# Optimization experiments

Measured on AMD Instinct MI355X. Metric: run time of the kernel, lower is better.

Reference implementation:

```python
import jax, jax.numpy as jnp
import numpy as np

N_NODES = 100_000
N_EDGES = 1_600_000
F_IN, F_HID, F_OUT = 128, 64, 128


def setup_inputs() -> dict:
    key = jax.random.key(0)
    k_x, k_e, k_w1, k_w2 = jax.random.split(key, 4)
    x = jax.random.normal(k_x, (N_NODES, F_IN), dtype=jnp.float32)
    edge_index = jax.random.randint(k_e, (2, N_EDGES), 0, N_NODES, dtype=jnp.int32)
    # Glorot-style init for the two GCN conv weight matrices
    W1 = jax.random.normal(k_w1, (F_IN, F_HID), dtype=jnp.float32) * (1.0 / np.sqrt(F_IN))
    b1 = jnp.zeros((F_HID,), dtype=jnp.float32)
    W2 = jax.random.normal(k_w2, (F_HID, F_OUT), dtype=jnp.float32) * (1.0 / np.sqrt(F_HID))
    b2 = jnp.zeros((F_OUT,), dtype=jnp.float32)
    return {"x": x, "edge_index": edge_index, "W1": W1, "b1": b1, "W2": W2, "b2": b2}


def _gcn_conv(x, W, b, src, dst, num_nodes):
    """GCNConv: out = D^{-1/2} (A + I) D^{-1/2} (x W) + b.
    Self-loops handled analytically: deg includes +1, and the self-loop
    message for node i is norm_i^2 * h_i."""
    h = x @ W  # [N, F_out]
    ones = jnp.ones(src.shape[0], dtype=h.dtype)
    deg = jax.ops.segment_sum(ones, dst, num_segments=num_nodes) + 1.0  # +1 self-loop
    norm = jax.lax.rsqrt(deg)  # [N]
    # gather source messages scaled by norm_src, scatter-add into dst
    agg = jax.ops.segment_sum(h[src] * norm[src, None], dst, num_segments=num_nodes)
    return norm[:, None] * agg + (norm * norm)[:, None] * h + b


def reference(x, edge_index, W1, b1, W2, b2):
    src, dst = edge_index[0], edge_index[1]
    n = x.shape[0]
    h = jax.nn.relu(_gcn_conv(x, W1, b1, src, dst, n))
    # dropout p=0.0 -> identity (module default)
    return _gcn_conv(h, W2, b2, src, dst, n)
```

## Files before the change

### kernel.cpp

```cpp
#include <hip/hip_runtime.h>
#include <hip/hip_bf16.h>

#define F_IN 128
#define F_HID 64
#define F_OUT 128
#define BSH 9
#define BS  (1 << BSH)
#define MAXNB 256

__device__ __forceinline__ int clampi(int v, int lo, int hi) {
    return v < lo ? lo : (v > hi ? hi : v);
}

__device__ __forceinline__ unsigned short f2bf(float f) {
    unsigned int u = __float_as_uint(f);
    u = (u + 0x7FFFu + ((u >> 16) & 1u)) >> 16;
    return (unsigned short)u;
}
__device__ __forceinline__ float bf2f(unsigned short s) {
    return __uint_as_float(((unsigned int)s) << 16);
}

__global__ void zero2_kernel(int* __restrict__ a, int* __restrict__ b, int n) {
    int i = blockIdx.x * blockDim.x + threadIdx.x;
    if (i < n) { a[i] = 0; b[i] = 0; }
}

__global__ void bhist_kernel(const int* __restrict__ dst, int* __restrict__ bhist,
                             int E, int Nn, int NB) {
    __shared__ int lh[MAXNB];
    for (int i = threadIdx.x; i < NB; i += 256) lh[i] = 0;
    __syncthreads();
    int chunk = (E + gridDim.x - 1) / gridDim.x;
    int base = blockIdx.x * chunk;
    int end = base + chunk; if (end > E) end = E;
    for (int i = base + threadIdx.x; i < end; i += 256) {
        int d = clampi(dst[i], 0, Nn - 1);
        atomicAdd(&lh[d >> BSH], 1);
    }
    __syncthreads();
    for (int i = threadIdx.x; i < NB; i += 256)
        if (lh[i]) atomicAdd(&bhist[i], lh[i]);
}

__device__ void bplace_body(int* lh, int* gb, int* bbuf, int lb, int NPL,
                            const int* __restrict__ src, const int* __restrict__ dst,
                            const int* __restrict__ bhist, int* __restrict__ bbase,
                            int* __restrict__ bcur, int* __restrict__ staging,
                            int E, int Nn, int NB) {
    int t = threadIdx.x;
    int v = (t < NB) ? bhist[t] : 0;
    bbuf[t] = v;
    __syncthreads();
    for (int dd = 1; dd < MAXNB; dd <<= 1) {
        int x = (t >= dd) ? bbuf[t - dd] : 0;
        __syncthreads();
        bbuf[t] += x;
        __syncthreads();
    }
    int excl = bbuf[t] - v;
    __syncthreads();
    bbuf[t] = excl;
    if (lb == 0 && t < NB) bbase[t] = excl;
    for (int i = t; i < NB; i += 256) lh[i] = 0;
    __syncthreads();

    int chunk = (E + NPL - 1) / NPL;
    int base = lb * chunk;
    int end = base + chunk; if (end > E) end = E;
    for (int i = base + t; i < end; i += 256) {
        int d = clampi(dst[i], 0, Nn - 1);
        atomicAdd(&lh[d >> BSH], 1);
    }
    __syncthreads();
    for (int i = t; i < NB; i += 256) {
        int c = lh[i];
        gb[i] = (c > 0) ? bbuf[i] + atomicAdd(&bcur[i], c) : 0;
        lh[i] = 0;
    }
    __syncthreads();
    for (int i = base + t; i < end; i += 256) {
        int d = clampi(dst[i], 0, Nn - 1);
        int s = clampi(src[i], 0, Nn - 1);
        int b = d >> BSH;
        int p = gb[b] + atomicAdd(&lh[b], 1);
        staging[p] = (s << BSH) | (d & (BS - 1));
    }
}

__global__ void bfine_kernel(const int* __restrict__ bhist, const int* __restrict__ bbase,
                             const int* __restrict__ staging,
                             int* __restrict__ cnt, int* __restrict__ off,
                             float* __restrict__ nrm, int* __restrict__ csr, int Nn) {
    __shared__ int lcnt[BS];
    __shared__ int loff[BS];
    __shared__ int lcur[BS];
    __shared__ int ps[256];
    int b = blockIdx.x;
    int t = threadIdx.x;
    int base  = bbase[b];
    int count = bhist[b];
    int node0 = b << BSH;

    for (int r = t; r < BS; r += 256) lcnt[r] = 0;
    __syncthreads();
    for (int i = t; i < count; i += 256)
        atomicAdd(&lcnt[staging[base + i] & (BS - 1)], 1);
    __syncthreads();

    int a0 = lcnt[2 * t], a1 = lcnt[2 * t + 1];
    int pair = a0 + a1;
    ps[t] = pair;
    __syncthreads();
    for (int d = 1; d < 256; d <<= 1) {
        int x = (t >= d) ? ps[t - d] : 0;
        __syncthreads();
        ps[t] += x;
        __syncthreads();
    }
    int excl = ps[t] - pair;
    loff[2 * t]     = excl;
    loff[2 * t + 1] = excl + a0;
    __syncthreads();

    for (int r = t; r < BS; r += 256) {
        int node = node0 + r;
        if (node < Nn) {
            int c = lcnt[r];
            cnt[node] = c;
            off[node] = base + loff[r];
            nrm[node] = rsqrtf((float)c + 1.0f);
        }
        lcur[r] = 0;
    }
    __syncthreads();

    for (int i = t; i < count; i += 256) {
        int v = staging[base + i];
        int r = v & (BS - 1);
        int p = base + loff[r] + atomicAdd(&lcur[r], 1);
        csr[p] = v >> BSH;
    }
}

template<int K, int N, bool BIAS, bool BF16OUT>
__device__ void gemm_body(float* __restrict__ Ws, int lb,
                          const float* __restrict__ A, const float* __restrict__ B,
                          const float* __restrict__ bias,
                          void* __restrict__ Cv, int M) {
    constexpr int CT = N / 8;
    constexpr int RB = (256 / CT) * 4;

    int tid = threadIdx.x;
    for (int i = tid; i < K * N / 4; i += 256)
        ((float4*)Ws)[i] = ((const float4*)B)[i];
    __syncthreads();

    int ct = tid % CT;
    int rt = tid / CT;
    int row0 = lb * RB + rt * 4;
    int c0 = ct * 8;

    float acc[4][8];
#pragma unroll
    for (int r = 0; r < 4; r++)
#pragma unroll
        for (int c = 0; c < 8; c++) acc[r][c] = 0.f;

    for (int kk = 0; kk < K; kk += 8) {
        float4 av[4], av2[4];
#pragma unroll
        for (int r = 0; r < 4; r++) {
            int row = row0 + r;
            if (row < M) {
                av[r]  = *(const float4*)(A + (size_t)row * K + kk);
                av2[r] = *(const float4*)(A + (size_t)row * K + kk + 4);
            } else {
                av[r]  = make_float4(0.f, 0.f, 0.f, 0.f);
                av2[r] = make_float4(0.f, 0.f, 0.f, 0.f);
            }
        }
#pragma unroll
        for (int j = 0; j < 4; j++) {
            const float* wrow = Ws + (kk + j) * N + c0;
            float4 w0 = *(const float4*)(wrow);
            float4 w1 = *(const float4*)(wrow + 4);
            float wj[8] = {w0.x, w0.y, w0.z, w0.w, w1.x, w1.y, w1.z, w1.w};
#pragma unroll
            for (int r = 0; r < 4; r++) {
                float a = (j == 0) ? av[r].x : (j == 1) ? av[r].y : (j == 2) ? av[r].z : av[r].w;
#pragma unroll
                for (int c = 0; c < 8; c++)
                    acc[r][c] = fmaf(a, wj[c], acc[r][c]);
            }
        }
#pragma unroll
        for (int j = 0; j < 4; j++) {
            const float* wrow = Ws + (kk + 4 + j) * N + c0;
            float4 w0 = *(const float4*)(wrow);
            float4 w1 = *(const float4*)(wrow + 4);
            float wj[8] = {w0.x, w0.y, w0.z, w0.w, w1.x, w1.y, w1.z, w1.w};
#pragma unroll
            for (int r = 0; r < 4; r++) {
                float a = (j == 0) ? av2[r].x : (j == 1) ? av2[r].y : (j == 2) ? av2[r].z : av2[r].w;
#pragma unroll
                for (int c = 0; c < 8; c++)
                    acc[r][c] = fmaf(a, wj[c], acc[r][c]);
            }
        }
    }

    float bcol[8];
    if (BIAS) {
        float4 bb0 = *(const float4*)(bias + c0);
        float4 bb1 = *(const float4*)(bias + c0 + 4);
        bcol[0]=bb0.x; bcol[1]=bb0.y; bcol[2]=bb0.z; bcol[3]=bb0.w;
        bcol[4]=bb1.x; bcol[5]=bb1.y; bcol[6]=bb1.z; bcol[7]=bb1.w;
    }

#pragma unroll
    for (int r = 0; r < 4; r++) {
        int row = row0 + r;
        if (row >= M) continue;
        float o[8];
#pragma unroll
        for (int c = 0; c < 8; c++) {
            float v = acc[r][c];
            if (BIAS) v += bcol[c];
            o[c] = v;
        }
        if (BF16OUT) {
            unsigned int pk0 = (unsigned int)f2bf(o[0]) | ((unsigned int)f2bf(o[1]) << 16);
            unsigned int pk1 = (unsigned int)f2bf(o[2]) | ((unsigned int)f2bf(o[3]) << 16);
            unsigned int pk2 = (unsigned int)f2bf(o[4]) | ((unsigned int)f2bf(o[5]) << 16);
            unsigned int pk3 = (unsigned int)f2bf(o[6]) | ((unsigned int)f2bf(o[7]) << 16);
            uint4 pk; pk.x = pk0; pk.y = pk1; pk.z = pk2; pk.w = pk3;
            *(uint4*)((unsigned short*)Cv + (size_t)row * N + c0) = pk;
        } else {
            float4 o0, o1;
            o0.x = o[0]; o0.y = o[1]; o0.z = o[2]; o0.w = o[3];
            o1.x = o[4]; o1.y = o[5]; o1.z = o[6]; o1.w = o[7];
            float* crow = (float*)Cv + (size_t)row * N + c0;
            *(float4*)(crow) = o0;
            *(float4*)(crow + 4) = o1;
        }
    }
}

template<int K, int N, bool BIAS, bool BF16OUT>
__global__ void gemm_tiled(const float* __restrict__ A, const float* __restrict__ B,
                           const float* __restrict__ bias,
                           void* __restrict__ Cv, int M) {
    __shared__ float Ws[K * N];
    gemm_body<K, N, BIAS, BF16OUT>(Ws, blockIdx.x, A, B, bias, Cv, M);
}

__global__ void gemm1_bplace_kernel(const float* __restrict__ x, const float* __restrict__ W1,
                                    unsigned short* __restrict__ h1, int M, int NG,
                                    const int* __restrict__ src, const int* __restrict__ dst,
                                    const int* __restrict__ bhist, int* __restrict__ bbase,
                                    int* __restrict__ bcur, int* __restrict__ staging,
                                    int E, int Nn, int NB, int NPL) {
    __shared__ union SmA {
        float ws[F_IN * F_HID];
        struct { int lh[MAXNB]; int gb[MAXNB]; int bb[MAXNB]; } pl;
    } sm;
    if ((int)blockIdx.x < NG) {
        gemm_body<F_IN, F_HID, false, true>(sm.ws, blockIdx.x, x, W1, nullptr, h1, M);
    } else {
        bplace_body(sm.pl.lh, sm.pl.gb, sm.pl.bb, blockIdx.x - NG, NPL,
                    src, dst, bhist, bbase, bcur, staging, E, Nn, NB);
    }
}

__global__ void gather64_conv_kernel(const unsigned short* __restrict__ h,
                                     const float* __restrict__ norm,
                                     const int* __restrict__ off, const int* __restrict__ cnt,
                                     const int* __restrict__ csr_src,
                                     const float* __restrict__ bias,
                                     unsigned short* __restrict__ outp, int Nn, int E) {
    int wave = (blockIdx.x * blockDim.x + threadIdx.x) >> 6;
    int lane = threadIdx.x & 63;
    int node = __builtin_amdgcn_readfirstlane(wave);
    if (node >= Nn) return;

    int o0 = __builtin_amdgcn_readfirstlane(off[node]);
    int c  = __builtin_amdgcn_readfirstlane(cnt[node]);
    if (c < 0) c = 0;
    if (o0 < 0) o0 = 0;
    if (o0 + c > E) c = E - o0;

    const int* ce = csr_src + o0;
    float sum = 0.0f;
    int e = 0;
    for (; e + 16 <= c; e += 16) {
        int si[16];
        float nw[16];
        unsigned short v[16];
#pragma unroll
        for (int u = 0; u < 16; u++) si[u] = clampi(ce[e + u], 0, Nn - 1);
#pragma unroll
        for (int u = 0; u < 16; u++) nw[u] = norm[si[u]];
#pragma unroll
        for (int u = 0; u < 16; u++) v[u] = h[(size_t)si[u] * 64 + lane];
#pragma unroll
        for (int u = 0; u < 16; u++) sum = fmaf(nw[u], bf2f(v[u]), sum);
    }
    for (; e + 8 <= c; e += 8) {
        int si[8];
        float nw[8];
        unsigned short v[8];
#pragma unroll
        for (int u = 0; u < 8; u++) si[u] = clampi(ce[e + u], 0, Nn - 1);
#pragma unroll
        for (int u = 0; u < 8; u++) nw[u] = norm[si[u]];
#pragma unroll
        for (int u = 0; u < 8; u++) v[u] = h[(size_t)si[u] * 64 + lane];
#pragma unroll
        for (int u = 0; u < 8; u++) sum = fmaf(nw[u], bf2f(v[u]), sum);
    }
    for (; e + 4 <= c; e += 4) {
        int si[4];
        float nw[4];
        unsigned short v[4];
#pragma unroll
        for (int u = 0; u < 4; u++) si[u] = clampi(ce[e + u], 0, Nn - 1);
#pragma unroll
        for (int u = 0; u < 4; u++) nw[u] = norm[si[u]];
#pragma unroll
        for (int u = 0; u < 4; u++) v[u] = h[(size_t)si[u] * 64 + lane];
#pragma unroll
        for (int u = 0; u < 4; u++) sum = fmaf(nw[u], bf2f(v[u]), sum);
    }
    for (; e < c; e++) {
        int s = clampi(ce[e], 0, Nn - 1);
        sum = fmaf(norm[s], bf2f(h[(size_t)s * 64 + lane]), sum);
    }
    float self = bf2f(h[(size_t)node * 64 + lane]);
    float nv = norm[node];
    float r = nv * (sum + nv * self);
    r = nv * fmaxf(r + bias[lane], 0.0f);
    outp[(size_t)node * 64 + lane] = f2bf(r);
}

__global__ void gather64_plain_kernel(const unsigned short* __restrict__ h,
                                      const float* __restrict__ norm,
                                      const int* __restrict__ off, const int* __restrict__ cnt,
                                      const int* __restrict__ csr_src,
                                      float* __restrict__ outq, int Nn, int E) {
    int wave = (blockIdx.x * blockDim.x + threadIdx.x) >> 6;
    int lane = threadIdx.x & 63;
    int node = __builtin_amdgcn_readfirstlane(wave);
    if (node >= Nn) return;

    int o0 = __builtin_amdgcn_readfirstlane(off[node]);
    int c  = __builtin_amdgcn_readfirstlane(cnt[node]);
    if (c < 0) c = 0;
    if (o0 < 0) o0 = 0;
    if (o0 + c > E) c = E - o0;

    const int* ce = csr_src + o0;
    float sum = 0.0f;
    int e = 0;
    for (; e + 16 <= c; e += 16) {
        int si[16];
        unsigned short v[16];
#pragma unroll
        for (int u = 0; u < 16; u++) si[u] = clampi(ce[e + u], 0, Nn - 1);
#pragma unroll
        for (int u = 0; u < 16; u++) v[u] = h[(size_t)si[u] * 64 + lane];
#pragma unroll
        for (int u = 0; u < 16; u++) sum += bf2f(v[u]);
    }
    for (; e + 8 <= c; e += 8) {
        int si[8];
        unsigned short v[8];
#pragma unroll
        for (int u = 0; u < 8; u++) si[u] = clampi(ce[e + u], 0, Nn - 1);
#pragma unroll
        for (int u = 0; u < 8; u++) v[u] = h[(size_t)si[u] * 64 + lane];
#pragma unroll
        for (int u = 0; u < 8; u++) sum += bf2f(v[u]);
    }
    for (; e + 4 <= c; e += 4) {
        int si[4];
        unsigned short v[4];
#pragma unroll
        for (int u = 0; u < 4; u++) si[u] = clampi(ce[e + u], 0, Nn - 1);
#pragma unroll
        for (int u = 0; u < 4; u++) v[u] = h[(size_t)si[u] * 64 + lane];
#pragma unroll
        for (int u = 0; u < 4; u++) sum += bf2f(v[u]);
    }
    for (; e < c; e++) {
        int s = clampi(ce[e], 0, Nn - 1);
        sum += bf2f(h[(size_t)s * 64 + lane]);
    }
    float self = bf2f(h[(size_t)node * 64 + lane]);
    float nv = norm[node];
    outq[(size_t)node * 64 + lane] = nv * (sum + self);
}

extern "C" void kernel_launch(void* const* d_in, const int* in_sizes, int n_in,
                              void* d_out, int out_size, void* d_ws, size_t ws_size,
                              hipStream_t stream) {
    if (n_in < 6) return;
    const float* x   = (const float*)d_in[0];
    const int*   ei  = (const int*)d_in[1];
    const float* W1  = (const float*)d_in[2];
    const float* b1  = (const float*)d_in[3];
    const float* W2  = (const float*)d_in[4];
    const float* b2  = (const float*)d_in[5];
    float*       out = (float*)d_out;

    int Nn = in_sizes[0] / F_IN;
    int E  = in_sizes[1] / 2;
    const int* src = ei;
    const int* dst = ei + E;

    int NB = (Nn + BS - 1) >> BSH;
    if (NB > MAXNB) return;
    if (Nn > (1 << (31 - BSH))) return;

    size_t o = 0;
    auto alloc = [&](size_t bytes) { size_t cur = o; o += (bytes + 255) & ~(size_t)255; return cur; };
    size_t o_cnt   = alloc((size_t)Nn * 4);
    size_t o_off   = alloc((size_t)Nn * 4);
    size_t o_nrm   = alloc((size_t)Nn * 4);
    size_t o_csr   = alloc((size_t)E * 4);
    size_t o_stg   = alloc((size_t)E * 4);
    size_t o_bh    = alloc(MAXNB * 4);
    size_t o_bb    = alloc(MAXNB * 4);
    size_t o_bc    = alloc(MAXNB * 4);
    size_t o_h     = alloc((size_t)Nn * F_HID * 4);
    if (o > ws_size) return;

    char* ws = (char*)d_ws;
    int*   cnt   = (int*)(ws + o_cnt);
    int*   off   = (int*)(ws + o_off);
    float* nrm   = (float*)(ws + o_nrm);
    int*   csr   = (int*)(ws + o_csr);
    int*   stg   = (int*)(ws + o_stg);
    int*   bh    = (int*)(ws + o_bh);
    int*   bb    = (int*)(ws + o_bb);
    int*   bc    = (int*)(ws + o_bc);
    unsigned short* h1 = (unsigned short*)(ws + o_h);
    float*          q  = (float*)(ws + o_h);
    unsigned short* p  = (unsigned short*)(out + (size_t)Nn * F_HID);

    zero2_kernel<<<1, 256, 0, stream>>>(bh, bc, MAXNB);
    bhist_kernel<<<256, 256, 0, stream>>>(dst, bh, E, Nn, NB);
    int G1 = (Nn + 127) / 128;
    gemm1_bplace_kernel<<<G1 + 256, 256, 0, stream>>>(
        x, W1, h1, Nn, G1,
        src, dst, bh, bb, bc, stg, E, Nn, NB, 256);
    bfine_kernel<<<NB, 256, 0, stream>>>(bh, bb, stg, cnt, off, nrm, csr, Nn);

    gather64_conv_kernel<<<(Nn + 3) / 4, 256, 0, stream>>>(
        h1, nrm, off, cnt, csr, b1, p, Nn, E);

    gather64_plain_kernel<<<(Nn + 3) / 4, 256, 0, stream>>>(
        p, nrm, off, cnt, csr, q, Nn, E);
    {
        constexpr int RB = (256 / (F_OUT / 8)) * 4;
        gemm_tiled<F_HID, F_OUT, true, false><<<(Nn + RB - 1) / RB, 256, 0, stream>>>(
            q, W2, b2, out, Nn);
    }
}
```

Baseline: 320.6 us.

## Split first GEMM across placement and fine-bucket kernels to overlap CSR build

Splits the first-layer GEMM into two halves. One half is co-scheduled with the bucket placement pass and the other with the fine CSR build, which is now a device function inside a combined kernel. This fills idle CUs during the small bfine launch and hides GEMM work behind graph preprocessing. The zero kernel becomes a hipMemsetAsync, and the histogram grid is doubled. The fused kernel's shared memory is sized for the GEMM tile, which may limit occupancy for the bfine blocks.

After: 354.0 us. 10.4% more time.

```diff
diff --git a/kernel.cpp b/kernel.cpp
--- a/kernel.cpp
+++ b/kernel.cpp
@@ -19,11 +19,6 @@
 }
 __device__ __forceinline__ float bf2f(unsigned short s) {
     return __uint_as_float(((unsigned int)s) << 16);
-}
-
-__global__ void zero2_kernel(int* __restrict__ a, int* __restrict__ b, int n) {
-    int i = blockIdx.x * blockDim.x + threadIdx.x;
-    if (i < n) { a[i] = 0; b[i] = 0; }
 }
 
 __global__ void bhist_kernel(const int* __restrict__ dst, int* __restrict__ bhist,
@@ -88,15 +83,11 @@
     }
 }
 
-__global__ void bfine_kernel(const int* __restrict__ bhist, const int* __restrict__ bbase,
-                             const int* __restrict__ staging,
-                             int* __restrict__ cnt, int* __restrict__ off,
-                             float* __restrict__ nrm, int* __restrict__ csr, int Nn) {
-    __shared__ int lcnt[BS];
-    __shared__ int loff[BS];
-    __shared__ int lcur[BS];
-    __shared__ int ps[256];
-    int b = blockIdx.x;
+__device__ void bfine_body(int* lcnt, int* loff, int* lcur, int* ps, int b,
+                           const int* __restrict__ bhist, const int* __restrict__ bbase,
+                           const int* __restrict__ staging,
+                           int* __restrict__ cnt, int* __restrict__ off,
+                           float* __restrict__ nrm, int* __restrict__ csr, int Nn) {
     int t = threadIdx.x;
     int base  = bbase[b];
     int count = bhist[b];
@@ -255,12 +246,12 @@
     gemm_body<K, N, BIAS, BF16OUT>(Ws, blockIdx.x, A, B, bias, Cv, M);
 }
 
-__global__ void gemm1_bplace_kernel(const float* __restrict__ x, const float* __restrict__ W1,
-                                    unsigned short* __restrict__ h1, int M, int NG,
-                                    const int* __restrict__ src, const int* __restrict__ dst,
-                                    const int* __restrict__ bhist, int* __restrict__ bbase,
-                                    int* __restrict__ bcur, int* __restrict__ staging,
-                                    int E, int Nn, int NB, int NPL) {
+__global__ void gemm1a_bplace_kernel(const float* __restrict__ x, const float* __restrict__ W1,
+                                     unsigned short* __restrict__ h1, int M, int NG,
+                                     const int* __restrict__ src, const int* __restrict__ dst,
+                                     const int* __restrict__ bhist, int* __restrict__ bbase,
+                                     int* __restrict__ bcur, int* __restrict__ staging,
+                                     int E, int Nn, int NB, int NPL) {
     __shared__ union SmA {
         float ws[F_IN * F_HID];
         struct { int lh[MAXNB]; int gb[MAXNB]; int bb[MAXNB]; } pl;
@@ -270,6 +261,24 @@
     } else {
         bplace_body(sm.pl.lh, sm.pl.gb, sm.pl.bb, blockIdx.x - NG, NPL,
                     src, dst, bhist, bbase, bcur, staging, E, Nn, NB);
+    }
+}
+
+__global__ void gemm1b_bfine_kernel(const float* __restrict__ x, const float* __restrict__ W1,
+                                    unsigned short* __restrict__ h1, int M, int ROW0, int NG2,
+                                    const int* __restrict__ bhist, const int* __restrict__ bbase,
+                                    const int* __restrict__ staging,
+                                    int* __restrict__ cnt, int* __restrict__ off,
+                                    float* __restrict__ nrm, int* __restrict__ csr, int Nn) {
+    __shared__ union SmB {
+        float ws[F_IN * F_HID];
+        struct { int lcnt[BS]; int loff[BS]; int lcur[BS]; int ps[256]; } f;
+    } sm;
+    if ((int)blockIdx.x < NG2) {
+        gemm_body<F_IN, F_HID, false, true>(sm.ws, blockIdx.x + ROW0, x, W1, nullptr, h1, M);
+    } else {
+        bfine_body(sm.f.lcnt, sm.f.loff, sm.f.lcur, sm.f.ps, blockIdx.x - NG2,
+                   bhist, bbase, staging, cnt, off, nrm, csr, Nn);
     }
 }
 
@@ -448,13 +457,17 @@
     float*          q  = (float*)(ws + o_h);
     unsigned short* p  = (unsigned short*)(out + (size_t)Nn * F_HID);
 
-    zero2_kernel<<<1, 256, 0, stream>>>(bh, bc, MAXNB);
-    bhist_kernel<<<256, 256, 0, stream>>>(dst, bh, E, Nn, NB);
-    int G1 = (Nn + 127) / 128;
-    gemm1_bplace_kernel<<<G1 + 256, 256, 0, stream>>>(
-        x, W1, h1, Nn, G1,
+    hipMemsetAsync(ws + o_bh, 0, 3 * MAXNB * 4, stream);
+    bhist_kernel<<<512, 256, 0, stream>>>(dst, bh, E, Nn, NB);
+    int G1  = (Nn + 127) / 128;
+    int G1A = G1 / 2;
+    int G1B = G1 - G1A;
+    gemm1a_bplace_kernel<<<G1A + 256, 256, 0, stream>>>(
+        x, W1, h1, Nn, G1A,
         src, dst, bh, bb, bc, stg, E, Nn, NB, 256);
-    bfine_kernel<<<NB, 256, 0, stream>>>(bh, bb, stg, cnt, off, nrm, csr, Nn);
+    gemm1b_bfine_kernel<<<G1B + NB, 256, 0, stream>>>(
+        x, W1, h1, Nn, G1A, G1B,
+        bh, bb, stg, cnt, off, nrm, csr, Nn);
 
     gather64_conv_kernel<<<(Nn + 3) / 4, 256, 0, stream>>>(
         h1, nrm, off, cnt, csr, b1, p, Nn, E);
```
